# Performance work log

Hardware: AMD Instinct MI355X
Metric: run time of the kernel (lower is better)

## Reference

```python
import jax, jax.numpy as jnp
import numpy as np

SR = 44100
SHORT_TAU_MS = 50.0
LONG_TAU_MS = 3000.0


def ms2coef(ms, sr):
    return float(1.0 - np.exp(-2200.0 / (ms * sr)))


C_SHORT = ms2coef(SHORT_TAU_MS, SR)
C_LONG = ms2coef(LONG_TAU_MS, SR)
ALIGN_SHIFT = int(SR * (LONG_TAU_MS - SHORT_TAU_MS) * 0.0005)  # 65047


def _ema(x, coef):
    """One-pole EMA along last axis: y[t] = coef*x[t] + (1-coef)*y[t-1], y[-1]=0.
    Implemented as a parallel (associative) scan over the linear recurrence."""
    a = jnp.full_like(x, 1.0 - coef)
    b = coef * x

    def combine(l, r):
        a1, b1 = l
        a2, b2 = r
        return (a1 * a2, a2 * b1 + b2)

    _, y = jax.lax.associative_scan(combine, (a, b), axis=-1)
    return y


def _ldr(x):
    # flatten leading dims, then log(short EMA) - log(rolled long EMA)
    x = x.reshape(-1, x.shape[-1])
    short = _ema(x, C_SHORT)
    long_ = jnp.roll(_ema(x, C_LONG), -ALIGN_SHIFT, axis=-1)
    return jnp.log(short) - jnp.log(long_)


def setup_inputs() -> dict:
    key = jax.random.key(0)
    k1, k2 = jax.random.split(key)
    B, T = 16, 1048576
    # squared signals: strictly positive (tiny offset avoids log(0) at t=0)
    pred_sq = jax.random.uniform(k1, (B, T), dtype=jnp.float32) + 1e-6
    target_sq = jax.random.uniform(k2, (B, T), dtype=jnp.float32) + 1e-6
    return {"pred_sq": pred_sq, "target_sq": target_sq}


def reference(pred_sq, target_sq):
    return jnp.mean(jnp.abs(_ldr(pred_sq) - _ldr(target_sq)))
```

## Files before the change

kernel.cpp:

```cpp
#include <hip/hip_runtime.h>
#include <math.h>

#define TPB   256
#define SL    16
#define SEGS  65536
#define PAIRS 32768
#define TLEN  1048576
#define MOFF  4065
#define ROFF  7
#define NEMA  4
#define TILE  1024
#define NTILE 64

typedef float v4f __attribute__((ext_vector_type(4)));

__device__ __forceinline__ float comp(const float4& v, int m) {
    return m == 0 ? v.x : m == 1 ? v.y : m == 2 ? v.z : v.w;
}

__device__ __forceinline__ float ipowf(float base, int e) {
    float r = 1.0f, p = base;
    while (e) { if (e & 1) r *= p; p *= p; e >>= 1; }
    return r;
}

__global__ __launch_bounds__(TPB) void ldr_partials(
    const float* __restrict__ pred, const float* __restrict__ targ,
    float amS, float amL, float* __restrict__ pB, int rows)
{
    const int tid = blockIdx.x * TPB + threadIdx.x;
    const int r = tid / PAIRS;
    const int p = tid & (PAIRS - 1);
    const size_t base = (size_t)r * TLEN + (size_t)p * 32;
    const float* P = pred + base;
    const float* T = targ + base;

    v4f u0, u1, u2, u3, u4, u5, u6, u7;
    v4f w0, w1, w2, w3, w4, w5, w6, w7;
    asm volatile(
        "global_load_dwordx4 %[u0], %[pa], off\n\t"
        "global_load_dwordx4 %[u1], %[pa], off offset:16\n\t"
        "global_load_dwordx4 %[u2], %[pa], off offset:32\n\t"
        "global_load_dwordx4 %[u3], %[pa], off offset:48\n\t"
        "global_load_dwordx4 %[u4], %[pa], off offset:64\n\t"
        "global_load_dwordx4 %[u5], %[pa], off offset:80\n\t"
        "global_load_dwordx4 %[u6], %[pa], off offset:96\n\t"
        "global_load_dwordx4 %[u7], %[pa], off offset:112\n\t"
        "global_load_dwordx4 %[w0], %[ta], off\n\t"
        "global_load_dwordx4 %[w1], %[ta], off offset:16\n\t"
        "global_load_dwordx4 %[w2], %[ta], off offset:32\n\t"
        "global_load_dwordx4 %[w3], %[ta], off offset:48\n\t"
        "global_load_dwordx4 %[w4], %[ta], off offset:64\n\t"
        "global_load_dwordx4 %[w5], %[ta], off offset:80\n\t"
        "global_load_dwordx4 %[w6], %[ta], off offset:96\n\t"
        "global_load_dwordx4 %[w7], %[ta], off offset:112\n\t"
        "s_waitcnt vmcnt(0)"
        : [u0] "=&v"(u0), [u1] "=&v"(u1), [u2] "=&v"(u2), [u3] "=&v"(u3),
          [u4] "=&v"(u4), [u5] "=&v"(u5), [u6] "=&v"(u6), [u7] "=&v"(u7),
          [w0] "=&v"(w0), [w1] "=&v"(w1), [w2] "=&v"(w2), [w3] "=&v"(w3),
          [w4] "=&v"(w4), [w5] "=&v"(w5), [w6] "=&v"(w6), [w7] "=&v"(w7)
        : [pa] "v"(P), [ta] "v"(T)
        : "memory");

    float res[NEMA][2];
    #define PQ(Q) { sp = fmaf(amS, sp, Q.x); lp = fmaf(amL, lp, Q.x);         \
                    sp = fmaf(amS, sp, Q.y); lp = fmaf(amL, lp, Q.y);         \
                    sp = fmaf(amS, sp, Q.z); lp = fmaf(amL, lp, Q.z);         \
                    sp = fmaf(amS, sp, Q.w); lp = fmaf(amL, lp, Q.w); }
    #define TQ(Q) { st = fmaf(amS, st, Q.x); lt = fmaf(amL, lt, Q.x);         \
                    st = fmaf(amS, st, Q.y); lt = fmaf(amL, lt, Q.y);         \
                    st = fmaf(amS, st, Q.z); lt = fmaf(amL, lt, Q.z);         \
                    st = fmaf(amS, st, Q.w); lt = fmaf(amL, lt, Q.w); }
    {
        float sp = 0.f, st = 0.f, lp = 0.f, lt = 0.f;
        PQ(u0) PQ(u1) PQ(u2) PQ(u3)
        TQ(w0) TQ(w1) TQ(w2) TQ(w3)
        res[0][0] = sp; res[1][0] = st; res[2][0] = lp; res[3][0] = lt;
    }
    {
        float sp = 0.f, st = 0.f, lp = 0.f, lt = 0.f;
        PQ(u4) PQ(u5) PQ(u6) PQ(u7)
        TQ(w4) TQ(w5) TQ(w6) TQ(w7)
        res[0][1] = sp; res[1][1] = st; res[2][1] = lp; res[3][1] = lt;
    }
    #undef PQ
    #undef TQ
    const size_t plane = (size_t)rows * SEGS;
    const size_t idx = (size_t)r * SEGS + 2 * (size_t)p;
    #pragma unroll
    for (int E = 0; E < NEMA; ++E)
        *(float2*)(pB + E * plane + idx) = make_float2(res[E][0], res[E][1]);
}

__global__ __launch_bounds__(TPB) void ldr_tile_agg(
    const float* __restrict__ pB, float* __restrict__ tA,
    float AcS, float AcL, int rows)
{
    __shared__ float slots[4];
    const int t = blockIdx.x, g = blockIdx.y;
    const int j = threadIdx.x, lane = j & 63, w = j >> 6;
    const float Ac = (g < 2 * rows) ? AcS : AcL;
    const float Ac4 = (Ac * Ac) * (Ac * Ac);
    const float4 E = *(const float4*)(pB + (size_t)g * SEGS
                                      + (size_t)t * TILE + (size_t)j * 4);
    float B = E.x;
    B = fmaf(Ac, B, E.y); B = fmaf(Ac, B, E.z); B = fmaf(Ac, B, E.w);
    float incl = B, Ad = Ac4;
    #pragma unroll
    for (int d = 1; d < 64; d <<= 1) {
        float pb = __shfl_up(incl, d, 64);
        if (lane >= d) incl = fmaf(Ad, pb, incl);
        Ad *= Ad;
    }
    if (lane == 63) slots[w] = incl;
    __syncthreads();
    if (j == 0) {
        const float Ac256 = ipowf(Ac4, 64);
        float T = slots[0];
        T = fmaf(Ac256, T, slots[1]);
        T = fmaf(Ac256, T, slots[2]);
        T = fmaf(Ac256, T, slots[3]);
        tA[g * NTILE + t] = T;
    }
}

__global__ __launch_bounds__(64) void ldr_tile_scan(
    const float* __restrict__ tA, float* __restrict__ tC,
    float AtS, float AtL, int rows)
{
    const int g = blockIdx.x, lane = threadIdx.x;
    const float A = (g < 2 * rows) ? AtS : AtL;
    float incl = tA[g * NTILE + lane], Ad = A;
    #pragma unroll
    for (int d = 1; d < 64; d <<= 1) {
        float pb = __shfl_up(incl, d, 64);
        if (lane >= d) incl = fmaf(Ad, pb, incl);
        Ad *= Ad;
    }
    float ex = __shfl_up(incl, 1, 64);
    if (lane == 0) ex = 0.f;
    tC[g * NTILE + lane] = ex;
}

__global__ __launch_bounds__(TPB) void ldr_carry_fill(
    float* __restrict__ pB, const float* __restrict__ tC,
    float AcS, float AcL, float Ac256S, float Ac256L, int rows)
{
    __shared__ float slots[4];
    const int t = blockIdx.x, g = blockIdx.y;
    const int j = threadIdx.x, lane = j & 63, w = j >> 6;
    const bool isShort = g < 2 * rows;
    const float Ac    = isShort ? AcS : AcL;
    const float Ac4   = (Ac * Ac) * (Ac * Ac);
    const float Ac256 = isShort ? Ac256S : Ac256L;
    float* ptr = pB + (size_t)g * SEGS + (size_t)t * TILE + (size_t)j * 4;
    const float4 E = *(const float4*)ptr;
    float B = E.x;
    B = fmaf(Ac, B, E.y); B = fmaf(Ac, B, E.z); B = fmaf(Ac, B, E.w);
    float incl = B, Ad = Ac4;
    #pragma unroll
    for (int d = 1; d < 64; d <<= 1) {
        float pb = __shfl_up(incl, d, 64);
        if (lane >= d) incl = fmaf(Ad, pb, incl);
        Ad *= Ad;
    }
    float ex = __shfl_up(incl, 1, 64);
    if (lane == 0) ex = 0.f;
    if (lane == 63) slots[w] = incl;
    __syncthreads();
    float acc = tC[g * NTILE + t];
    for (int u = 0; u < w; ++u) acc = fmaf(acc, Ac256, slots[u]);
    float carry = fmaf(ipowf(Ac4, lane), acc, ex);
    float4 out;
    out.x = carry; carry = fmaf(Ac, carry, E.x);
    out.y = carry; carry = fmaf(Ac, carry, E.y);
    out.z = carry; carry = fmaf(Ac, carry, E.z);
    out.w = carry;
    *(float4*)ptr = out;
}

__global__ __launch_bounds__(TPB) void ldr_loss(
    const float* __restrict__ pred, const float* __restrict__ targ,
    const float* __restrict__ cin,
    float amS, float amL, float* __restrict__ partial, int rows)
{
    __shared__ float rs[4];
    const int tid = blockIdx.x * TPB + threadIdx.x;
    const int lane = threadIdx.x & 63, w = threadIdx.x >> 6;
    const int r = tid >> 16, m = tid & (SEGS - 1);
    const int a = (m + MOFF) & (SEGS - 1);
    const int b = (m + MOFF + 1) & (SEGS - 1);
    const float* P = pred + (size_t)r * TLEN;
    const float* T = targ + (size_t)r * TLEN;
    const size_t plane = (size_t)rows * SEGS;
    const size_t rbase = (size_t)r * SEGS;

    float sp[SL], st[SL];
    {
        const float4* Sp4 = (const float4*)(P + (size_t)m * SL);
        const float4* St4 = (const float4*)(T + (size_t)m * SL);
        float ysp = cin[0 * plane + rbase + m];
        float yst = cin[1 * plane + rbase + m];
        #pragma unroll
        for (int q = 0; q < SL / 4; ++q) {
            float4 u = Sp4[q], v = St4[q];
            #pragma unroll
            for (int mm = 0; mm < 4; ++mm) {
                ysp = fmaf(amS, ysp, comp(u, mm)); sp[4 * q + mm] = ysp;
                yst = fmaf(amS, yst, comp(v, mm)); st[4 * q + mm] = yst;
            }
        }
    }

    float ylp = cin[2 * plane + rbase + a];
    float ylt = cin[3 * plane + rbase + a];
    const float4* Ap4 = (const float4*)(P + (size_t)a * SL);
    const float4* At4 = (const float4*)(T + (size_t)a * SL);
    const float4* Bp4 = (const float4*)(P + (size_t)b * SL);
    const float4* Bt4 = (const float4*)(T + (size_t)b * SL);

    float lsum = 0.f;
    #pragma unroll
    for (int q = 0; q < SL / 4; ++q) {
        float4 u = Ap4[q], v = At4[q];
        #pragma unroll
        for (int mm = 0; mm < 4; ++mm) {
            const int e = 4 * q + mm;
            ylp = fmaf(amL, ylp, comp(u, mm));
            ylt = fmaf(amL, ylt, comp(v, mm));
            if (e >= ROFF) {
                const int i = e - ROFF;
                lsum += fabsf(__logf(__fdividef(sp[i] * ylt, st[i] * ylp)));
            }
        }
    }
    #pragma unroll
    for (int q = 0; q < 2; ++q) {
        float4 u = Bp4[q], v = Bt4[q];
        #pragma unroll
        for (int mm = 0; mm < 4; ++mm) {
            const int e = 4 * q + mm;
            if (e < ROFF) {
                ylp = fmaf(amL, ylp, comp(u, mm));
                ylt = fmaf(amL, ylt, comp(v, mm));
                const int i = e + (SL - ROFF);
                lsum += fabsf(__logf(__fdividef(sp[i] * ylt, st[i] * ylp)));
            }
        }
    }

    #pragma unroll
    for (int d = 32; d > 0; d >>= 1) lsum += __shfl_xor(lsum, d, 64);
    if (lane == 0) rs[w] = lsum;
    __syncthreads();
    if (threadIdx.x == 0)
        partial[blockIdx.x] = rs[0] + rs[1] + rs[2] + rs[3];
}

__global__ void ldr_finalize(const float* __restrict__ partial, int nparts,
                             float* __restrict__ out, double inv_n)
{
    __shared__ double sd[256];
    double s = 0.0;
    for (int i = threadIdx.x; i < nparts; i += 256) s += (double)partial[i];
    sd[threadIdx.x] = s;
    __syncthreads();
    for (int d = 128; d > 0; d >>= 1) {
        if (threadIdx.x < d) sd[threadIdx.x] += sd[threadIdx.x + d];
        __syncthreads();
    }
    if (threadIdx.x == 0) out[0] = (float)(sd[0] * inv_n);
}

extern "C" void kernel_launch(void* const* d_in, const int* in_sizes, int n_in,
                              void* d_out, int out_size, void* d_ws, size_t ws_size,
                              hipStream_t stream)
{
    const float* pred = (const float*)d_in[0];
    const float* targ = (const float*)d_in[1];
    const int n = in_sizes[0];
    const int rows = n / TLEN;

    const double csd = 1.0 - exp(-2200.0 / (50.0 * 44100.0));
    const double cld = 1.0 - exp(-2200.0 / (3000.0 * 44100.0));
    const double amSd = 1.0 - csd, amLd = 1.0 - cld;
    const float amS = (float)amSd, amL = (float)amLd;
    const float AcS    = (float)pow(amSd, 16.0);
    const float AcL    = (float)pow(amLd, 16.0);
    const float Ac256S = (float)pow(amSd, 16.0 * 256);
    const float Ac256L = (float)pow(amLd, 16.0 * 256);
    const float AtS    = (float)pow(amSd, 16.0 * TILE);
    const float AtL    = (float)pow(amLd, 16.0 * TILE);

    char* wsb = (char*)d_ws;
    float* pB      = (float*)(wsb + 256);
    float* partial = pB + (size_t)NEMA * rows * SEGS;
    float* tA      = partial + 4096;
    float* tC      = tA + NEMA * 16 * NTILE;

    const int nthreads = rows * SEGS;
    const int nblocksL = nthreads / TPB;
    const int nblocksP = rows * PAIRS / TPB;
    const int nplanes  = NEMA * rows;

    ldr_partials<<<nblocksP, TPB, 0, stream>>>(pred, targ, amS, amL, pB, rows);
    dim3 gridT(NTILE, nplanes);
    ldr_tile_agg<<<gridT, TPB, 0, stream>>>(pB, tA, AcS, AcL, rows);
    ldr_tile_scan<<<nplanes, 64, 0, stream>>>(tA, tC, AtS, AtL, rows);
    ldr_carry_fill<<<gridT, TPB, 0, stream>>>(pB, tC, AcS, AcL,
                                              Ac256S, Ac256L, rows);
    ldr_loss<<<nblocksL, TPB, 0, stream>>>(pred, targ, pB, amS, amL,
                                           partial, rows);

    const double inv_n = 1.0 / ((double)rows * (double)TLEN);
    ldr_finalize<<<1, 256, 0, stream>>>(partial, nblocksL, (float*)d_out, inv_n);
}
```

Measured before the change: 80.20 us.

## Fuse tile aggregation into partials and in-block carry scan into loss kernel

Tile aggregates (256 tiles per row) are now computed as a weighted reduction at the end of the partials kernel. The separate tile_agg and carry_fill passes are removed, and the loss kernel rebuilds per-segment carries locally from the segment aggregates and the tile-level exclusive prefixes. This cuts two kernel launches plus a read/write pass over the carry buffer. In exchange the loss kernel does extra shuffle scans, shared-memory staging for the shifted long-EMA window, and an ipowf-weighted sum whose float accuracy differs from the old approach.

New measurement: 76.40 us. 4.7% less time.

```diff
diff --git a/kernel.cpp b/kernel.cpp
--- a/kernel.cpp
+++ b/kernel.cpp
@@ -9,8 +9,7 @@
 #define MOFF  4065
 #define ROFF  7
 #define NEMA  4
-#define TILE  1024
-#define NTILE 64
+#define TPL   256
 
 typedef float v4f __attribute__((ext_vector_type(4)));
 
@@ -26,10 +25,14 @@
 
 __global__ __launch_bounds__(TPB) void ldr_partials(
     const float* __restrict__ pred, const float* __restrict__ targ,
-    float amS, float amL, float* __restrict__ pB, int rows)
-{
-    const int tid = blockIdx.x * TPB + threadIdx.x;
-    const int r = tid / PAIRS;
+    float amS, float amL, float Ac16S, float Ac16L,
+    float* __restrict__ pB, float* __restrict__ tA, int rows)
+{
+    __shared__ float wt[4][NEMA];
+    const int b = blockIdx.x, j = threadIdx.x;
+    const int lane = j & 63, w = j >> 6;
+    const int tid = b * TPB + j;
+    const int r = tid >> 15;
     const int p = tid & (PAIRS - 1);
     const size_t base = (size_t)r * TLEN + (size_t)p * 32;
     const float* P = pred + base;
@@ -90,117 +93,158 @@
     #pragma unroll
     for (int E = 0; E < NEMA; ++E)
         *(float2*)(pB + E * plane + idx) = make_float2(res[E][0], res[E][1]);
-}
-
-__global__ __launch_bounds__(TPB) void ldr_tile_agg(
-    const float* __restrict__ pB, float* __restrict__ tA,
-    float AcS, float AcL, int rows)
-{
-    __shared__ float slots[4];
-    const int t = blockIdx.x, g = blockIdx.y;
-    const int j = threadIdx.x, lane = j & 63, w = j >> 6;
-    const float Ac = (g < 2 * rows) ? AcS : AcL;
-    const float Ac4 = (Ac * Ac) * (Ac * Ac);
-    const float4 E = *(const float4*)(pB + (size_t)g * SEGS
-                                      + (size_t)t * TILE + (size_t)j * 4);
-    float B = E.x;
-    B = fmaf(Ac, B, E.y); B = fmaf(Ac, B, E.z); B = fmaf(Ac, B, E.w);
-    float incl = B, Ad = Ac4;
+
+    const int h = j & 127;
+    const float Ac32S = Ac16S * Ac16S, Ac32L = Ac16L * Ac16L;
+    const float wgtS = ipowf(Ac32S, 127 - h);
+    const float wgtL = ipowf(Ac32L, 127 - h);
+    #pragma unroll
+    for (int E = 0; E < NEMA; ++E) {
+        const float Ac16 = (E < 2) ? Ac16S : Ac16L;
+        const float wgt  = (E < 2) ? wgtS : wgtL;
+        float c = fmaf(Ac16, res[E][0], res[E][1]) * wgt;
+        #pragma unroll
+        for (int d = 32; d > 0; d >>= 1) c += __shfl_xor(c, d, 64);
+        if (lane == 0) wt[w][E] = c;
+    }
+    __syncthreads();
+    if (j == 0) {
+        const int lt0 = (b & 127) << 1;
+        #pragma unroll
+        for (int E = 0; E < NEMA; ++E) {
+            float* tp = tA + ((size_t)E * rows + r) * TPL;
+            tp[lt0]     = wt[0][E] + wt[1][E];
+            tp[lt0 + 1] = wt[2][E] + wt[3][E];
+        }
+    }
+}
+
+__global__ __launch_bounds__(64) void ldr_tile_scan(
+    const float* __restrict__ tA, float* __restrict__ tC,
+    float AcT_S, float AcT_L, int rows)
+{
+    const int g = blockIdx.x, lane = threadIdx.x;
+    const float AcT = (g < 2 * rows) ? AcT_S : AcT_L;
+    const float AcT4 = ((AcT * AcT) * (AcT * AcT));
+    const float* Bv = tA + (size_t)g * TPL + lane * 4;
+    float b4[4];
+    float B = 0.f;
+    #pragma unroll
+    for (int m = 0; m < 4; ++m) { b4[m] = Bv[m]; B = fmaf(AcT, B, b4[m]); }
+    float incl = B, Ad = AcT4;
     #pragma unroll
     for (int d = 1; d < 64; d <<= 1) {
         float pb = __shfl_up(incl, d, 64);
         if (lane >= d) incl = fmaf(Ad, pb, incl);
         Ad *= Ad;
     }
-    if (lane == 63) slots[w] = incl;
-    __syncthreads();
-    if (j == 0) {
-        const float Ac256 = ipowf(Ac4, 64);
-        float T = slots[0];
-        T = fmaf(Ac256, T, slots[1]);
-        T = fmaf(Ac256, T, slots[2]);
-        T = fmaf(Ac256, T, slots[3]);
-        tA[g * NTILE + t] = T;
-    }
-}
-
-__global__ __launch_bounds__(64) void ldr_tile_scan(
-    const float* __restrict__ tA, float* __restrict__ tC,
-    float AtS, float AtL, int rows)
-{
-    const int g = blockIdx.x, lane = threadIdx.x;
-    const float A = (g < 2 * rows) ? AtS : AtL;
-    float incl = tA[g * NTILE + lane], Ad = A;
-    #pragma unroll
-    for (int d = 1; d < 64; d <<= 1) {
-        float pb = __shfl_up(incl, d, 64);
-        if (lane >= d) incl = fmaf(Ad, pb, incl);
-        Ad *= Ad;
-    }
-    float ex = __shfl_up(incl, 1, 64);
-    if (lane == 0) ex = 0.f;
-    tC[g * NTILE + lane] = ex;
-}
-
-__global__ __launch_bounds__(TPB) void ldr_carry_fill(
-    float* __restrict__ pB, const float* __restrict__ tC,
-    float AcS, float AcL, float Ac256S, float Ac256L, int rows)
-{
-    __shared__ float slots[4];
-    const int t = blockIdx.x, g = blockIdx.y;
-    const int j = threadIdx.x, lane = j & 63, w = j >> 6;
-    const bool isShort = g < 2 * rows;
-    const float Ac    = isShort ? AcS : AcL;
-    const float Ac4   = (Ac * Ac) * (Ac * Ac);
-    const float Ac256 = isShort ? Ac256S : Ac256L;
-    float* ptr = pB + (size_t)g * SEGS + (size_t)t * TILE + (size_t)j * 4;
-    const float4 E = *(const float4*)ptr;
-    float B = E.x;
-    B = fmaf(Ac, B, E.y); B = fmaf(Ac, B, E.z); B = fmaf(Ac, B, E.w);
-    float incl = B, Ad = Ac4;
-    #pragma unroll
-    for (int d = 1; d < 64; d <<= 1) {
-        float pb = __shfl_up(incl, d, 64);
-        if (lane >= d) incl = fmaf(Ad, pb, incl);
-        Ad *= Ad;
-    }
-    float ex = __shfl_up(incl, 1, 64);
-    if (lane == 0) ex = 0.f;
-    if (lane == 63) slots[w] = incl;
-    __syncthreads();
-    float acc = tC[g * NTILE + t];
-    for (int u = 0; u < w; ++u) acc = fmaf(acc, Ac256, slots[u]);
-    float carry = fmaf(ipowf(Ac4, lane), acc, ex);
-    float4 out;
-    out.x = carry; carry = fmaf(Ac, carry, E.x);
-    out.y = carry; carry = fmaf(Ac, carry, E.y);
-    out.z = carry; carry = fmaf(Ac, carry, E.z);
-    out.w = carry;
-    *(float4*)ptr = out;
+    float carry = __shfl_up(incl, 1, 64);
+    if (lane == 0) carry = 0.f;
+    float* co = tC + (size_t)g * TPL + lane * 4;
+    #pragma unroll
+    for (int m = 0; m < 4; ++m) {
+        co[m] = carry;
+        carry = fmaf(AcT, carry, b4[m]);
+    }
 }
 
 __global__ __launch_bounds__(TPB) void ldr_loss(
     const float* __restrict__ pred, const float* __restrict__ targ,
-    const float* __restrict__ cin,
-    float amS, float amL, float* __restrict__ partial, int rows)
-{
+    const float* __restrict__ pB, const float* __restrict__ tC,
+    float amS, float amL, float Ac16S, float Ac16L,
+    float* __restrict__ partial, int rows)
+{
+    __shared__ float sS[2][4], sL[2][4];
+    __shared__ float longC[2][512];
     __shared__ float rs[4];
-    const int tid = blockIdx.x * TPB + threadIdx.x;
-    const int lane = threadIdx.x & 63, w = threadIdx.x >> 6;
-    const int r = tid >> 16, m = tid & (SEGS - 1);
+    const int bgl = blockIdx.x;
+    const int r = bgl >> 8, bl = bgl & 255;
+    const int j = threadIdx.x, lane = j & 63, w = j >> 6;
+    const int m = bl * 256 + j;
+    const size_t plane = (size_t)rows * SEGS;
+    const size_t rbase = (size_t)r * SEGS;
+
+    const float A1024S = ipowf(Ac16S, 64);
+    const float aLaneS = ipowf(Ac16S, lane);
+    float aggS[2];
+    aggS[0] = pB[0 * plane + rbase + m];
+    aggS[1] = pB[1 * plane + rbase + m];
+    float inS0 = aggS[0], inS1 = aggS[1], Ad = Ac16S;
+    #pragma unroll
+    for (int d = 1; d < 64; d <<= 1) {
+        float p0 = __shfl_up(inS0, d, 64);
+        float p1 = __shfl_up(inS1, d, 64);
+        if (lane >= d) { inS0 = fmaf(Ad, p0, inS0); inS1 = fmaf(Ad, p1, inS1); }
+        Ad *= Ad;
+    }
+    float exS0 = __shfl_up(inS0, 1, 64), exS1 = __shfl_up(inS1, 1, 64);
+    if (lane == 0) { exS0 = 0.f; exS1 = 0.f; }
+    if (lane == 63) { sS[0][w] = inS0; sS[1][w] = inS1; }
+
+    const int half = j >> 7;
+    const int hh = j & 127;
+    const int tsel = (bl + 15 + half) & 255;
+    const float Ac32L = Ac16L * Ac16L;
+    const float A2048L = ipowf(Ac32L, 64);
+    const float aLaneL = ipowf(Ac32L, lane);
+    float2 agL0 = *(const float2*)(pB + 2 * plane + rbase + tsel * 256 + 2 * hh);
+    float2 agL1 = *(const float2*)(pB + 3 * plane + rbase + tsel * 256 + 2 * hh);
+    float pa0 = fmaf(Ac16L, agL0.x, agL0.y);
+    float pa1 = fmaf(Ac16L, agL1.x, agL1.y);
+    float inL0 = pa0, inL1 = pa1;
+    Ad = Ac32L;
+    #pragma unroll
+    for (int d = 1; d < 64; d <<= 1) {
+        float p0 = __shfl_up(inL0, d, 64);
+        float p1 = __shfl_up(inL1, d, 64);
+        if (lane >= d) { inL0 = fmaf(Ad, p0, inL0); inL1 = fmaf(Ad, p1, inL1); }
+        Ad *= Ad;
+    }
+    float exL0 = __shfl_up(inL0, 1, 64), exL1 = __shfl_up(inL1, 1, 64);
+    if (lane == 0) { exL0 = 0.f; exL1 = 0.f; }
+    if (lane == 63) { sL[0][w] = inL0; sL[1][w] = inL1; }
+    __syncthreads();
+
+    {
+        const float baseS0 = tC[((size_t)0 * rows + r) * TPL + bl];
+        const float baseS1 = tC[((size_t)1 * rows + r) * TPL + bl];
+        float Wc0 = 0.f, Wc1 = 0.f;
+        for (int u = 0; u < w; ++u) {
+            Wc0 = fmaf(Wc0, A1024S, sS[0][u]);
+            Wc1 = fmaf(Wc1, A1024S, sS[1][u]);
+        }
+        const float aThS = aLaneS * ipowf(A1024S, w);
+        exS0 = fmaf(aThS, baseS0, fmaf(aLaneS, Wc0, exS0));
+        exS1 = fmaf(aThS, baseS1, fmaf(aLaneS, Wc1, exS1));
+    }
+    {
+        const float baseL0 = tC[((size_t)2 * rows + r) * TPL + tsel];
+        const float baseL1 = tC[((size_t)3 * rows + r) * TPL + tsel];
+        const int hw = w & 1, fw = w & 2;
+        float Wc0 = hw ? sL[0][fw] : 0.f;
+        float Wc1 = hw ? sL[1][fw] : 0.f;
+        const float aThL = aLaneL * (hw ? A2048L : 1.f);
+        float c00 = fmaf(aThL, baseL0, fmaf(aLaneL, Wc0, exL0));
+        float c10 = fmaf(aThL, baseL1, fmaf(aLaneL, Wc1, exL1));
+        const int i0 = half * 256 + 2 * hh;
+        longC[0][i0] = c00; longC[0][i0 + 1] = fmaf(Ac16L, c00, agL0.x);
+        longC[1][i0] = c10; longC[1][i0 + 1] = fmaf(Ac16L, c10, agL1.x);
+    }
+    __syncthreads();
+    const float cSp = exS0, cSt = exS1;
+    const float cLp = longC[0][225 + j];
+    const float cLt = longC[1][225 + j];
+
     const int a = (m + MOFF) & (SEGS - 1);
-    const int b = (m + MOFF + 1) & (SEGS - 1);
+    const int bseg = (m + MOFF + 1) & (SEGS - 1);
     const float* P = pred + (size_t)r * TLEN;
     const float* T = targ + (size_t)r * TLEN;
-    const size_t plane = (size_t)rows * SEGS;
-    const size_t rbase = (size_t)r * SEGS;
 
     float sp[SL], st[SL];
     {
         const float4* Sp4 = (const float4*)(P + (size_t)m * SL);
         const float4* St4 = (const float4*)(T + (size_t)m * SL);
-        float ysp = cin[0 * plane + rbase + m];
-        float yst = cin[1 * plane + rbase + m];
+        float ysp = cSp, yst = cSt;
         #pragma unroll
         for (int q = 0; q < SL / 4; ++q) {
             float4 u = Sp4[q], v = St4[q];
@@ -211,13 +255,11 @@
             }
         }
     }
-
-    float ylp = cin[2 * plane + rbase + a];
-    float ylt = cin[3 * plane + rbase + a];
+    float ylp = cLp, ylt = cLt;
     const float4* Ap4 = (const float4*)(P + (size_t)a * SL);
     const float4* At4 = (const float4*)(T + (size_t)a * SL);
-    const float4* Bp4 = (const float4*)(P + (size_t)b * SL);
-    const float4* Bt4 = (const float4*)(T + (size_t)b * SL);
+    const float4* Bp4 = (const float4*)(P + (size_t)bseg * SL);
+    const float4* Bt4 = (const float4*)(T + (size_t)bseg * SL);
 
     float lsum = 0.f;
     #pragma unroll
@@ -253,8 +295,7 @@
     for (int d = 32; d > 0; d >>= 1) lsum += __shfl_xor(lsum, d, 64);
     if (lane == 0) rs[w] = lsum;
     __syncthreads();
-    if (threadIdx.x == 0)
-        partial[blockIdx.x] = rs[0] + rs[1] + rs[2] + rs[3];
+    if (j == 0) partial[bgl] = rs[0] + rs[1] + rs[2] + rs[3];
 }
 
 __global__ void ldr_finalize(const float* __restrict__ partial, int nparts,
@@ -285,32 +326,26 @@
     const double cld = 1.0 - exp(-2200.0 / (3000.0 * 44100.0));
     const double amSd = 1.0 - csd, amLd = 1.0 - cld;
     const float amS = (float)amSd, amL = (float)amLd;
-    const float AcS    = (float)pow(amSd, 16.0);
-    const float AcL    = (float)pow(amLd, 16.0);
-    const float Ac256S = (float)pow(amSd, 16.0 * 256);
-    const float Ac256L = (float)pow(amLd, 16.0 * 256);
-    const float AtS    = (float)pow(amSd, 16.0 * TILE);
-    const float AtL    = (float)pow(amLd, 16.0 * TILE);
+    const float Ac16S = (float)pow(amSd, 16.0);
+    const float Ac16L = (float)pow(amLd, 16.0);
+    const float AcT_S = (float)pow(amSd, 4096.0);
+    const float AcT_L = (float)pow(amLd, 4096.0);
 
     char* wsb = (char*)d_ws;
     float* pB      = (float*)(wsb + 256);
-    float* partial = pB + (size_t)NEMA * rows * SEGS;
-    float* tA      = partial + 4096;
-    float* tC      = tA + NEMA * 16 * NTILE;
-
-    const int nthreads = rows * SEGS;
-    const int nblocksL = nthreads / TPB;
+    float* tA      = pB + (size_t)NEMA * rows * SEGS;
+    float* tC      = tA + (size_t)NEMA * rows * TPL;
+    float* partial = tC + (size_t)NEMA * rows * TPL;
+
     const int nblocksP = rows * PAIRS / TPB;
+    const int nblocksL = rows * TPL;
     const int nplanes  = NEMA * rows;
 
-    ldr_partials<<<nblocksP, TPB, 0, stream>>>(pred, targ, amS, amL, pB, rows);
-    dim3 gridT(NTILE, nplanes);
-    ldr_tile_agg<<<gridT, TPB, 0, stream>>>(pB, tA, AcS, AcL, rows);
-    ldr_tile_scan<<<nplanes, 64, 0, stream>>>(tA, tC, AtS, AtL, rows);
-    ldr_carry_fill<<<gridT, TPB, 0, stream>>>(pB, tC, AcS, AcL,
-                                              Ac256S, Ac256L, rows);
-    ldr_loss<<<nblocksL, TPB, 0, stream>>>(pred, targ, pB, amS, amL,
-                                           partial, rows);
+    ldr_partials<<<nblocksP, TPB, 0, stream>>>(pred, targ, amS, amL,
+                                               Ac16S, Ac16L, pB, tA, rows);
+    ldr_tile_scan<<<nplanes, 64, 0, stream>>>(tA, tC, AcT_S, AcT_L, rows);
+    ldr_loss<<<nblocksL, TPB, 0, stream>>>(pred, targ, pB, tC, amS, amL,
+                                           Ac16S, Ac16L, partial, rows);
 
     const double inv_n = 1.0 / ((double)rows * (double)TLEN);
     ldr_finalize<<<1, 256, 0, stream>>>(partial, nblocksL, (float*)d_out, inv_n);
```
